# Optimization experiments

Hardware: AMD Instinct MI355X
Metric: run time of the kernel (lower is better)

## Reference

```python
import jax, jax.numpy as jnp
import numpy as np

# Dimensions: d_model D, heads H, head dim DH (H*DH==D), resonator freqs NF, FFN rank R
B, T, D, H, DH, NF, R = 2, 1024, 1024, 16, 64, 256, 4096
EPS_LN = 1e-5
EPS_ATTN = 1e-6


def setup_inputs() -> dict:
    key = jax.random.key(0)
    ks = jax.random.split(key, 16)
    n = lambda i, shape, s=0.02: jax.random.normal(ks[i], shape, dtype=jnp.float32) * s
    return {
        "x": jax.random.normal(ks[0], (B, T, D), dtype=jnp.float32),
        # resonator input projections
        "W_amp": n(1, (D, NF)), "b_amp": jnp.zeros((NF,), jnp.float32),
        "W_phi": n(2, (D, NF)), "b_phi": jnp.zeros((NF,), jnp.float32),
        # resonator dynamics: per-frequency rotation, retention logit, firing threshold
        "omega": jax.random.uniform(ks[3], (NF,), dtype=jnp.float32, minval=0.0, maxval=float(np.pi)),
        "ret_logit": jnp.full((NF,), 2.0, jnp.float32),
        "theta": jnp.full((NF,), 0.5, jnp.float32),
        # feat_proj: 3*NF -> D
        "W_feat": n(4, (3 * NF, D)), "b_feat": jnp.zeros((D,), jnp.float32),
        # linear attention projections (BDH-GPU style, relu feature map, no out proj)
        "Wq": n(5, (D, H * DH)), "Wk": n(6, (D, H * DH)), "Wv": n(7, (D, H * DH)),
        # per-head layernorm affine
        "lnh_w": jnp.ones((H, DH), jnp.float32), "lnh_b": jnp.zeros((H, DH), jnp.float32),
        # ReLU low-rank FFN (positive_out=True)
        "W1": n(8, (D, R)), "b1": jnp.zeros((R,), jnp.float32),
        "W2": n(9, (R, D)), "b2": jnp.zeros((D,), jnp.float32),
        # final layernorm
        "ln_w": jnp.ones((D,), jnp.float32), "ln_b": jnp.zeros((D,), jnp.float32),
    }


def reference(x, W_amp, b_amp, W_phi, b_phi, omega, ret_logit, theta,
              W_feat, b_feat, Wq, Wk, Wv, lnh_w, lnh_b,
              W1, b1, W2, b2, ln_w, ln_b):
    Bb, Tt, Dd = x.shape
    # --- resonator input field: complex polar(amp, phi) ---
    amp = jax.nn.softplus(x @ W_amp + b_amp)                 # [B,T,NF]
    phi = jnp.float32(np.pi) * jnp.tanh(x @ W_phi + b_phi)   # [B,T,NF]
    u = jax.lax.complex(amp * jnp.cos(phi), amp * jnp.sin(phi))  # complex64 [B,T,NF]
    # --- sequential complex resonator recurrence (the kernel-headroom scan) ---
    decay = jax.nn.sigmoid(ret_logit)                         # [NF]
    a = jax.lax.complex(decay * jnp.cos(omega), decay * jnp.sin(omega))  # [NF] complex

    def step(X, u_t):
        pre = a * X + u_t                                     # [B,NF] complex
        g = jax.nn.sigmoid(jnp.abs(pre) - theta)              # threshold-map gate
        Xn = pre * g.astype(pre.dtype)
        return Xn, Xn

    X0 = jnp.zeros((Bb, u.shape[-1]), jnp.complex64)
    _, Xs = jax.lax.scan(step, X0, jnp.swapaxes(u, 0, 1))     # [T,B,NF]
    Xs = jnp.swapaxes(Xs, 0, 1)                               # [B,T,NF]
    feat = jnp.concatenate([Xs.real, Xs.imag, jnp.abs(Xs)], axis=-1)  # [B,T,3NF]
    h = jax.nn.relu(feat @ W_feat + b_feat)                   # pos(feat_proj(feat)) -> [B,T,D]
    # --- causal linear attention (relu feature map, cumulative KV state) ---
    q = jax.nn.relu(h @ Wq).reshape(Bb, Tt, H, DH)
    k = jax.nn.relu(h @ Wk).reshape(Bb, Tt, H, DH)
    v = (h @ Wv).reshape(Bb, Tt, H, DH)
    kv = jnp.cumsum(k[..., :, None] * v[..., None, :], axis=1)  # [B,T,H,DH,DH]
    ksum = jnp.cumsum(k, axis=1)                                 # [B,T,H,DH]
    num = jnp.einsum('bthd,bthde->bthe', q, kv)
    den = jnp.einsum('bthd,bthd->bth', q, ksum)[..., None] + EPS_ATTN
    y = num / den                                                # [B,T,H,DH]
    # --- per-head layernorm ---
    mean = y.mean(-1, keepdims=True)
    var = y.var(-1, keepdims=True)
    y = (y - mean) / jnp.sqrt(var + EPS_LN) * lnh_w + lnh_b
    y = y.reshape(Bb, Tt, H * DH)                                # [B,T,D]
    # --- ReLU low-rank FFN, positive_out ---
    y = jax.nn.relu(jax.nn.relu(y @ W1 + b1) @ W2 + b2)
    # --- residual + layernorm ---
    z = x + y
    mu = z.mean(-1, keepdims=True)
    vz = z.var(-1, keepdims=True)
    out = (z - mu) / jnp.sqrt(vz + EPS_LN) * ln_w + ln_b
    return out
```

## Files before the change

kernel.cpp:

```cpp
#include <hip/hip_runtime.h>
#include <hip/hip_bf16.h>
#include <math.h>

#ifndef M_PI_F
#define M_PI_F 3.14159265358979323846f
#endif

static constexpr int Bb = 2, Tt = 1024, Dd = 1024, Hh = 16, DHh = 64, NFf = 256, Rr = 4096;
static constexpr int Mm = Bb * Tt;
static constexpr int CHK = 64, NCHK = Tt / CHK;
static constexpr int QS = 3072;

enum Epi { EPI_NONE = 0, EPI_RELU, EPI_QKV };

typedef __attribute__((ext_vector_type(8))) short bf16x8;
typedef __attribute__((ext_vector_type(4))) float f32x4;

__device__ inline float bf2f(unsigned short u) {
  union { unsigned int i; float f; } c;
  c.i = (unsigned int)u << 16;
  return c.f;
}

__device__ inline void gload16(const short* g, short* l) {
  __builtin_amdgcn_global_load_lds(
      (const __attribute__((address_space(1))) unsigned int*)g,
      (__attribute__((address_space(3))) unsigned int*)l, 16, 0, 0);
}

#define GSTAGE(bufsel, kk0)                                           \
  _Pragma("unroll") for (int si = 0; si < 4; ++si) {                  \
    const int s = wid + si * 4;                                       \
    gload16(A + (size_t)(m0 + s * 8 + srow) * ldk + (kk0) + skk,      \
            &lA[(bufsel) * 8192 + s * 512]);                          \
    gload16(BT + (size_t)(n0 + s * 8 + srow) * ldk + (kk0) + skk,     \
            &lB[(bufsel) * 8192 + s * 512]);                          \
  }

template <int EPI, int OUTBF, int SPLITK>
__global__ __launch_bounds__(256) void gemm_mfma(const short* __restrict__ A,
                                                 const short* __restrict__ BT,
                                                 const float* __restrict__ bias,
                                                 float* __restrict__ Cf,
                                                 __hip_bfloat16* __restrict__ Cb,
                                                 int M, int N, int ldk) {
  __shared__ short lA[2 * 128 * 64];
  __shared__ short lB[2 * 128 * 64];
  const int tid = threadIdx.x;
  const int wid = tid >> 6, lane = tid & 63;

  const int nwg = gridDim.x * gridDim.y;
  const int wg = blockIdx.y * gridDim.x + blockIdx.x;
  const int qq = nwg >> 3, rr = nwg & 7;
  const int xcd = wg & 7, idx = wg >> 3;
  const int wg2 = (xcd < rr ? xcd * (qq + 1) : rr * (qq + 1) + (xcd - rr) * qq) + idx;
  const int bx = wg2 % gridDim.x, by = wg2 / gridDim.x;

  const int m0 = by * 128, n0 = bx * 128;
  const int wm = (wid >> 1) * 64, wn = (wid & 1) * 64;
  const int srow = lane >> 3;
  const int skk = (((lane & 7) ^ (lane >> 3)) << 3);

  int kstart = 0, klen = ldk;
  if (SPLITK > 1) {
    klen = ldk / SPLITK;
    kstart = blockIdx.z * klen;
    if (OUTBF)
      Cb += (size_t)blockIdx.z * M * N;
    else
      Cf += (size_t)blockIdx.z * M * N;
  }
  const int kend = kstart + klen;

  f32x4 acc[4][4] = {};

  GSTAGE(0, kstart);
  int cur = 0;
  for (int k0 = kstart; k0 < kend; k0 += 64) {
    if (k0 + 64 < kend) {
      GSTAGE(cur ^ 1, k0 + 64);
      asm volatile("s_waitcnt vmcnt(8)" ::: "memory");
    } else {
      asm volatile("s_waitcnt vmcnt(0)" ::: "memory");
    }
    asm volatile("s_barrier" ::: "memory");
    const short* bA = &lA[cur * 8192];
    const short* bB = &lB[cur * 8192];
#pragma unroll
    for (int kk = 0; kk < 2; ++kk) {
      const int krd = kk * 32 + (lane >> 4) * 8;
      const int rsel = lane & 15;
      const int kswz = krd ^ ((rsel & 7) << 3);
      bf16x8 af[4], bfr[4];
#pragma unroll
      for (int i = 0; i < 4; ++i) {
        af[i] = *(const bf16x8*)&bA[(wm + i * 16 + rsel) * 64 + kswz];
        bfr[i] = *(const bf16x8*)&bB[(wn + i * 16 + rsel) * 64 + kswz];
      }
#pragma unroll
      for (int i = 0; i < 4; ++i)
#pragma unroll
        for (int j = 0; j < 4; ++j)
          acc[i][j] = __builtin_amdgcn_mfma_f32_16x16x32_bf16(af[i], bfr[j], acc[i][j], 0, 0, 0);
    }
    asm volatile("s_barrier" ::: "memory");
    cur ^= 1;
  }

  const int crow = (lane >> 4) * 4;
  const int ccol = lane & 15;
#pragma unroll
  for (int j = 0; j < 4; ++j) {
    const int col = n0 + wn + j * 16 + ccol;
    const float bv = bias ? bias[col] : 0.f;
#pragma unroll
    for (int i = 0; i < 4; ++i) {
#pragma unroll
      for (int r = 0; r < 4; ++r) {
        float v = acc[i][j][r] + bv;
        const int row = m0 + wm + i * 16 + crow + r;
        if (EPI == EPI_QKV) {
          const float vv = (col < 2048) ? fmaxf(v, 0.f) : v;
          Cb[(size_t)row * QS + col] = __float2bfloat16(vv);
        } else {
          if (EPI == EPI_RELU) v = fmaxf(v, 0.f);
          const size_t off = (size_t)row * N + col;
          if (OUTBF)
            Cb[off] = __float2bfloat16(v);
          else
            Cf[off] = v;
        }
      }
    }
  }
}

__device__ __forceinline__ void tc_tile(float (*tile)[33], const float* __restrict__ W,
                                        __hip_bfloat16* __restrict__ WT, int K, int N,
                                        int tlocal) {
  const int tilesN = N / 32;
  const int bk = (tlocal / tilesN) * 32, bn = (tlocal % tilesN) * 32;
  const int tx = threadIdx.x & 31, ty = threadIdx.x >> 5;
#pragma unroll
  for (int r = 0; r < 32; r += 8) tile[ty + r][tx] = W[(size_t)(bk + ty + r) * N + bn + tx];
  __syncthreads();
#pragma unroll
  for (int r = 0; r < 32; r += 8)
    WT[(size_t)(bn + ty + r) * K + bk + tx] = __float2bfloat16(tile[tx][ty + r]);
}

__global__ __launch_bounds__(256) void tc_first(const float* __restrict__ W_amp,
                                                const float* __restrict__ W_phi,
                                                __hip_bfloat16* __restrict__ WTamp,
                                                __hip_bfloat16* __restrict__ WTphi,
                                                const float* __restrict__ x,
                                                __hip_bfloat16* __restrict__ xb) {
  __shared__ float tile[32][33];
  const int bid = blockIdx.x;
  if (bid >= 512) {
    const int i = ((bid - 512) * 256 + threadIdx.x) * 4;
    const float4 v = *(const float4*)&x[i];
    xb[i + 0] = __float2bfloat16(v.x);
    xb[i + 1] = __float2bfloat16(v.y);
    xb[i + 2] = __float2bfloat16(v.z);
    xb[i + 3] = __float2bfloat16(v.w);
    return;
  }
  if (bid < 256)
    tc_tile(tile, W_amp, WTamp, 1024, 256, bid);
  else
    tc_tile(tile, W_phi, WTphi, 1024, 256, bid - 256);
}

__global__ __launch_bounds__(256) void reduce_polar(const __hip_bfloat16* __restrict__ part,
                                                    const float* __restrict__ b_amp,
                                                    const float* __restrict__ b_phi,
                                                    __hip_bfloat16* __restrict__ outr,
                                                    __hip_bfloat16* __restrict__ outi) {
  const int idx = blockIdx.x * 256 + threadIdx.x;
  const int row = idx >> 8, c = idx & 255;
  const size_t MN = (size_t)Mm * 512;
  const size_t pa = (size_t)row * 512 + c;
  const unsigned short* pu = (const unsigned short*)part;
  float a = bf2f(pu[pa]) + bf2f(pu[pa + MN]) + bf2f(pu[pa + 2 * MN]) + bf2f(pu[pa + 3 * MN]) +
            b_amp[c];
  float ph = bf2f(pu[pa + 256]) + bf2f(pu[pa + 256 + MN]) + bf2f(pu[pa + 256 + 2 * MN]) +
             bf2f(pu[pa + 256 + 3 * MN]) + b_phi[c];
  a = (a > 0.f) ? (a + log1pf(expf(-a))) : log1pf(expf(a));
  ph = M_PI_F * tanhf(ph);
  float s, co;
  sincosf(ph, &s, &co);
  outr[idx] = __float2bfloat16(a * co);
  outi[idx] = __float2bfloat16(a * s);
}

static constexpr int RES_P = 16;
static constexpr int RES_TC = 128;
static constexpr int RES_W = 128;

#define RES_LOAD(buf_r, buf_i, tg)                                        \
  if ((tg) < cend) {                                                      \
    _Pragma("unroll") for (int i = 0; i < RES_P; ++i) {                   \
      buf_r[i] = __bfloat162float(ur[bbase + (size_t)((tg) + i) * NFf]);  \
      buf_i[i] = __bfloat162float(ui[bbase + (size_t)((tg) + i) * NFf]);  \
    }                                                                     \
  }

#define RES_STEP(buf_r, buf_i, tg)                                      \
  {                                                                      \
    const bool wr_ = (tg) >= cstart;                                     \
    _Pragma("unroll") for (int i = 0; i < RES_P; ++i) {                  \
      const float pr = fmaf(ar, Xr, fmaf(-ai, Xi, buf_r[i]));            \
      const float pim = fmaf(ar, Xi, fmaf(ai, Xr, buf_i[i]));            \
      const float mag = __builtin_amdgcn_sqrtf(fmaf(pr, pr, pim * pim)); \
      const float g = __builtin_amdgcn_rcpf(1.f + __expf(th - mag));     \
      Xr = pr * g;                                                       \
      Xi = pim * g;                                                      \
      if (wr_) {                                                         \
        const size_t fb = ((size_t)b * Tt + (tg) + i) * (3 * NFf);       \
        featb[fb + f] = __float2bfloat16(Xr);                            \
        featb[fb + NFf + f] = __float2bfloat16(Xi);                      \
        featb[fb + 2 * NFf + f] = __float2bfloat16(mag * g);             \
      }                                                                  \
    }                                                                    \
  }

struct STDesc {
  const float* src[6];
  __hip_bfloat16* dst[6];
  const __hip_bfloat16* ur;
  const __hip_bfloat16* ui;
  const float* omega;
  const float* ret_logit;
  const float* theta;
  __hip_bfloat16* featb;
};

__global__ __launch_bounds__(256) void scan_and_tc(STDesc d) {
  __shared__ float tile[32][33];
  const int bid = blockIdx.x;
  if (bid < 64) {
    if (threadIdx.x >= 64) return;
    const int tc = bid & 7;
    const int fs = (bid >> 3) & 3;
    const int b = bid >> 5;
    const int f = fs * 64 + threadIdx.x;
    const int cstart = tc * RES_TC;
    const int cend = cstart + RES_TC;
    const int tbeg = (cstart >= RES_W) ? cstart - RES_W : 0;
    const __hip_bfloat16* ur = d.ur;
    const __hip_bfloat16* ui = d.ui;
    __hip_bfloat16* featb = d.featb;
    const float dec = 1.f / (1.f + __expf(-d.ret_logit[f]));
    float so, co;
    sincosf(d.omega[f], &so, &co);
    const float ar = dec * co, ai = dec * so;
    const float th = d.theta[f];
    const size_t bbase = (size_t)b * Tt * NFf + f;
    float Xr = 0.f, Xi = 0.f;
    float Ar[RES_P], Ai[RES_P], Br[RES_P], Bi[RES_P];
    RES_LOAD(Ar, Ai, tbeg);
    for (int t0 = tbeg; t0 < cend; t0 += 2 * RES_P) {
      RES_LOAD(Br, Bi, t0 + RES_P);
      RES_STEP(Ar, Ai, t0);
      RES_LOAD(Ar, Ai, t0 + 2 * RES_P);
      RES_STEP(Br, Bi, t0 + RES_P);
    }
    return;
  }
  constexpr int KS[6] = {768, 1024, 1024, 1024, 1024, 4096};
  constexpr int NS[6] = {1024, 1024, 1024, 1024, 4096, 1024};
  constexpr int CUM[7] = {0, 768, 1792, 2816, 3840, 7936, 12032};
  const int t = bid - 64;
  int w = 0;
#pragma unroll
  for (int i = 0; i < 6; ++i)
    if (t >= CUM[i + 1]) w = i + 1;
  tc_tile(tile, d.src[w], d.dst[w], KS[w], NS[w], t - CUM[w]);
}

__global__ __launch_bounds__(256) void attn_chunk_kv(const __hip_bfloat16* __restrict__ k,
                                                     const __hip_bfloat16* __restrict__ v,
                                                     __hip_bfloat16* __restrict__ S,
                                                     float* __restrict__ Ksum) {
  __shared__ float Ks[64][68], Vs[64][68];
  const int g = blockIdx.x;
  const int j = g & (NCHK - 1), bh = g >> 4;
  const int b = bh >> 4, h = bh & (Hh - 1);
  const int tid = threadIdx.x;
  const size_t rowbase = (size_t)(b * Tt + j * CHK) * QS + h * DHh;
  const unsigned short* ku = (const unsigned short*)k;
  const unsigned short* vu = (const unsigned short*)v;
  for (int l = tid; l < 4096; l += 256) {
    const int s = l >> 6, d = l & 63;
    Ks[s][d] = bf2f(ku[rowbase + (size_t)s * QS + d]);
    Vs[s][d] = bf2f(vu[rowbase + (size_t)s * QS + d]);
  }
  __syncthreads();
  const int d0 = tid & 63, eb = tid >> 6, e0 = eb * 16;
  float4 acc4[4] = {};
  float ks = 0.f;
  for (int s = 0; s < 64; ++s) {
    const float kd = Ks[s][d0];
    ks += kd;
#pragma unroll
    for (int i = 0; i < 4; ++i) {
      const float4 v4 = *(const float4*)&Vs[s][e0 + 4 * i];
      acc4[i].x = fmaf(kd, v4.x, acc4[i].x);
      acc4[i].y = fmaf(kd, v4.y, acc4[i].y);
      acc4[i].z = fmaf(kd, v4.z, acc4[i].z);
      acc4[i].w = fmaf(kd, v4.w, acc4[i].w);
    }
  }
  unsigned short* Sg = (unsigned short*)S + (size_t)g * 4096 + (size_t)d0 * 64 + e0;
#pragma unroll
  for (int i = 0; i < 4; ++i) {
    ushort4 o;
    __hip_bfloat16 h0 = __float2bfloat16(acc4[i].x);
    __hip_bfloat16 h1 = __float2bfloat16(acc4[i].y);
    __hip_bfloat16 h2 = __float2bfloat16(acc4[i].z);
    __hip_bfloat16 h3 = __float2bfloat16(acc4[i].w);
    o.x = *(unsigned short*)&h0;
    o.y = *(unsigned short*)&h1;
    o.z = *(unsigned short*)&h2;
    o.w = *(unsigned short*)&h3;
    *(ushort4*)&Sg[4 * i] = o;
  }
  if (eb == 0) Ksum[(size_t)g * 64 + d0] = ks;
}

__global__ __launch_bounds__(256) void attn_prefix(__hip_bfloat16* __restrict__ S,
                                                   float* __restrict__ Ksum) {
  const int bid = blockIdx.x;
  const int tid = threadIdx.x;
  if (bid < 512) {
    const int bh = bid >> 4, r = bid & 15;
    const int de = r * 256 + tid;
    unsigned short* Su = (unsigned short*)S;
    const size_t base = (size_t)bh * (NCHK * 4096) + de;
    float vv[NCHK];
#pragma unroll
    for (int j = 0; j < NCHK; ++j) vv[j] = bf2f(Su[base + (size_t)j * 4096]);
    float run = 0.f;
#pragma unroll
    for (int j = 0; j < NCHK; ++j) {
      const float tmp = vv[j];
      __hip_bfloat16 hv = __float2bfloat16(run);
      Su[base + (size_t)j * 4096] = *(unsigned short*)&hv;
      run += tmp;
    }
  } else {
    const int cid = (bid - 512) * 256 + tid;
    const int bh = cid >> 6, d = cid & 63;
    const size_t base = (size_t)bh * (NCHK * 64) + d;
    float vv[NCHK];
#pragma unroll
    for (int j = 0; j < NCHK; ++j) vv[j] = Ksum[base + (size_t)j * 64];
    float run = 0.f;
#pragma unroll
    for (int j = 0; j < NCHK; ++j) {
      const float tmp = vv[j];
      Ksum[base + (size_t)j * 64] = run;
      run += tmp;
    }
  }
}

__global__ __launch_bounds__(256) void attn_out(const __hip_bfloat16* __restrict__ q,
                                                const __hip_bfloat16* __restrict__ k,
                                                const __hip_bfloat16* __restrict__ v,
                                                const __hip_bfloat16* __restrict__ S,
                                                const float* __restrict__ Ksum,
                                                const float* __restrict__ lnw,
                                                const float* __restrict__ lnb,
                                                __hip_bfloat16* __restrict__ yhb) {
  __shared__ float Qs[64][68];
  __shared__ float KVP[64][68];
  __shared__ float At[64][66];
  __shared__ float denp[4][64];
  const int g = blockIdx.x;
  const int j = g & (NCHK - 1), bh = g >> 4;
  const int b = bh >> 4, h = bh & (Hh - 1);
  const int tid = threadIdx.x;
  const size_t rowbase = (size_t)(b * Tt + j * CHK) * QS + h * DHh;
  const unsigned short* qu = (const unsigned short*)q;
  const unsigned short* ku = (const unsigned short*)k;
  const unsigned short* vu = (const unsigned short*)v;
#define KSWZ(s, d) ((((d) >> 2) ^ (((s) >> 4) & 3)) * 4 + ((d) & 3))
  for (int l = tid; l < 4096; l += 256) {
    const int s = l >> 6, d = l & 63;
    Qs[s][d] = bf2f(qu[rowbase + (size_t)s * QS + d]);
    KVP[s][KSWZ(s, d)] = bf2f(vu[rowbase + (size_t)s * QS + d]);
  }
  {
    const int w4 = tid >> 6, ln = tid & 63;
    const int fr = ln & 15;
    const int kh = ln >> 4;
    const unsigned short* kr = ku + rowbase + (size_t)(w4 * 16 + fr) * QS + kh * 8;
    const bf16x8 a0 = *(const bf16x8*)&kr[0];
    const bf16x8 a1 = *(const bf16x8*)&kr[32];
    f32x4 accQK[4] = {};
#pragma unroll
    for (int tt = 0; tt < 4; ++tt) {
      const unsigned short* qr = qu + rowbase + (size_t)(tt * 16 + fr) * QS + kh * 8;
      const bf16x8 b0 = *(const bf16x8*)&qr[0];
      const bf16x8 b1 = *(const bf16x8*)&qr[32];
      accQK[tt] = __builtin_amdgcn_mfma_f32_16x16x32_bf16(a0, b0, accQK[tt], 0, 0, 0);
      accQK[tt] = __builtin_amdgcn_mfma_f32_16x16x32_bf16(a1, b1, accQK[tt], 0, 0, 0);
    }
#pragma unroll
    for (int tt = 0; tt < 4; ++tt) {
      const int t = tt * 16 + fr;
      float dp = 0.f;
#pragma unroll
      for (int r = 0; r < 4; ++r) {
        const int s = w4 * 16 + kh * 4 + r;
        const float val = (s <= t) ? accQK[tt][r] : 0.f;
        At[s][t] = val;
        dp += val;
      }
      dp += __shfl_xor(dp, 16);
      dp += __shfl_xor(dp, 32);
      if (ln < 16) denp[w4][t] = dp;
    }
  }
  __syncthreads();
  const int t = tid >> 2, sg = tid & 3;
  const float* pk = Ksum + (size_t)g * 64;
  float qpk = 0.f;
#pragma unroll
  for (int c = 0; c < 16; ++c) {
    const float4 q4 = *(const float4*)&Qs[t][4 * c];
    const float4 pk4 = *(const float4*)&pk[4 * c];
    qpk = fmaf(q4.x, pk4.x, fmaf(q4.y, pk4.y, fmaf(q4.z, pk4.z, fmaf(q4.w, pk4.w, qpk))));
  }
  const float den = denp[0][t] + denp[1][t] + denp[2][t] + denp[3][t] + qpk + 1e-6f;
  const int e0 = sg * 16;
  float4 num[4] = {};
  for (int s = 0; s <= t; ++s) {
    const float av = At[s][t];
    const int x = (s >> 4) & 3;
#pragma unroll
    for (int i = 0; i < 4; ++i) {
      const float4 v4 = *(const float4*)&KVP[s][e0 + 4 * (i ^ x)];
      num[i].x = fmaf(av, v4.x, num[i].x);
      num[i].y = fmaf(av, v4.y, num[i].y);
      num[i].z = fmaf(av, v4.z, num[i].z);
      num[i].w = fmaf(av, v4.w, num[i].w);
    }
  }
  __syncthreads();
  const unsigned short* Pg = (const unsigned short*)S + (size_t)g * 4096;
  for (int l = tid; l < 4096; l += 256) KVP[l >> 6][KSWZ(l >> 6, l & 63)] = bf2f(Pg[l]);
  __syncthreads();
  for (int d = 0; d < 64; ++d) {
    const float qd = Qs[t][d];
    const int x = (d >> 4) & 3;
#pragma unroll
    for (int i = 0; i < 4; ++i) {
      const float4 p4 = *(const float4*)&KVP[d][e0 + 4 * (i ^ x)];
      num[i].x = fmaf(qd, p4.x, num[i].x);
      num[i].y = fmaf(qd, p4.y, num[i].y);
      num[i].z = fmaf(qd, p4.z, num[i].z);
      num[i].w = fmaf(qd, p4.w, num[i].w);
    }
  }
#undef KSWZ
  const float inv = 1.f / den;
  float o[16];
#pragma unroll
  for (int i = 0; i < 4; ++i) {
    o[4 * i + 0] = num[i].x * inv;
    o[4 * i + 1] = num[i].y * inv;
    o[4 * i + 2] = num[i].z * inv;
    o[4 * i + 3] = num[i].w * inv;
  }
  float s1 = 0.f, s2 = 0.f;
#pragma unroll
  for (int i = 0; i < 16; ++i) {
    s1 += o[i];
    s2 += o[i] * o[i];
  }
  s1 += __shfl_xor(s1, 1);
  s1 += __shfl_xor(s1, 2);
  s2 += __shfl_xor(s2, 1);
  s2 += __shfl_xor(s2, 2);
  const float mean = s1 * (1.f / 64.f);
  const float var = s2 * (1.f / 64.f) - mean * mean;
  const float rsv = rsqrtf(var + 1e-5f);
  const float* wv = lnw + h * DHh + e0;
  const float* bv = lnb + h * DHh + e0;
  unsigned short ob[16];
#pragma unroll
  for (int i = 0; i < 16; ++i) {
    const float r = (o[i] - mean) * rsv * wv[i] + bv[i];
    __hip_bfloat16 hv = __float2bfloat16(r);
    ob[i] = *(unsigned short*)&hv;
  }
  unsigned short* yg =
      (unsigned short*)yhb + (size_t)(b * Tt + j * CHK + t) * Dd + h * DHh + e0;
#pragma unroll
  for (int i = 0; i < 4; ++i) *(ushort4*)&yg[4 * i] = *(ushort4*)&ob[4 * i];
}

__global__ __launch_bounds__(256) void final_ln(const float* __restrict__ x,
                                                const __hip_bfloat16* __restrict__ part,
                                                const float* __restrict__ b2,
                                                const float* __restrict__ w,
                                                const float* __restrict__ bb,
                                                float* __restrict__ out) {
  __shared__ float r1[4], r2[4];
  const int row = blockIdx.x;
  const int tid = threadIdx.x;
  const size_t off = (size_t)row * Dd + tid * 4;
  const size_t MN = (size_t)Mm * Dd;
  float acc4[4] = {0.f, 0.f, 0.f, 0.f};
#pragma unroll
  for (int z = 0; z < 4; ++z) {
    const ushort4 u = *(const ushort4*)&part[off + (size_t)z * MN];
    acc4[0] += bf2f(u.x);
    acc4[1] += bf2f(u.y);
    acc4[2] += bf2f(u.z);
    acc4[3] += bf2f(u.w);
  }
  const float4 bv = *(const float4*)&b2[tid * 4];
  const float4 xa = *(const float4*)&x[off];
  float z[4];
  z[0] = xa.x + fmaxf(acc4[0] + bv.x, 0.f);
  z[1] = xa.y + fmaxf(acc4[1] + bv.y, 0.f);
  z[2] = xa.z + fmaxf(acc4[2] + bv.z, 0.f);
  z[3] = xa.w + fmaxf(acc4[3] + bv.w, 0.f);
  float s1 = z[0] + z[1] + z[2] + z[3];
  float s2 = z[0] * z[0] + z[1] * z[1] + z[2] * z[2] + z[3] * z[3];
#pragma unroll
  for (int o = 1; o < 64; o <<= 1) {
    s1 += __shfl_xor(s1, o);
    s2 += __shfl_xor(s2, o);
  }
  const int wid = tid >> 6;
  if ((tid & 63) == 0) {
    r1[wid] = s1;
    r2[wid] = s2;
  }
  __syncthreads();
  const float t1 = r1[0] + r1[1] + r1[2] + r1[3];
  const float t2 = r2[0] + r2[1] + r2[2] + r2[3];
  const float mu = t1 * (1.f / Dd);
  const float var = t2 * (1.f / Dd) - mu * mu;
  const float rsv = rsqrtf(var + 1e-5f);
  float4 o4;
  float* op = &o4.x;
#pragma unroll
  for (int jj = 0; jj < 4; ++jj) op[jj] = (z[jj] - mu) * rsv * w[tid * 4 + jj] + bb[tid * 4 + jj];
  *(float4*)&out[off] = o4;
}

extern "C" void kernel_launch(void* const* d_in, const int* in_sizes, int n_in,
                              void* d_out, int out_size, void* d_ws, size_t ws_size,
                              hipStream_t stream) {
  const float* x = (const float*)d_in[0];
  const float* W_amp = (const float*)d_in[1];
  const float* b_amp = (const float*)d_in[2];
  const float* W_phi = (const float*)d_in[3];
  const float* b_phi = (const float*)d_in[4];
  const float* omega = (const float*)d_in[5];
  const float* ret_logit = (const float*)d_in[6];
  const float* theta = (const float*)d_in[7];
  const float* W_feat = (const float*)d_in[8];
  const float* b_feat = (const float*)d_in[9];
  const float* Wq = (const float*)d_in[10];
  const float* Wk = (const float*)d_in[11];
  const float* Wv = (const float*)d_in[12];
  const float* lnh_w = (const float*)d_in[13];
  const float* lnh_b = (const float*)d_in[14];
  const float* W1 = (const float*)d_in[15];
  const float* b1 = (const float*)d_in[16];
  const float* W2 = (const float*)d_in[17];
  const float* b2 = (const float*)d_in[18];
  const float* ln_w = (const float*)d_in[19];
  const float* ln_b = (const float*)d_in[20];

  char* p = (char*)d_ws;
  auto alloc = [&](size_t bytes) {
    char* r = p;
    p += (bytes + 255) & ~(size_t)255;
    return r;
  };
  __hip_bfloat16* xb = (__hip_bfloat16*)alloc((size_t)Mm * Dd * 2);
  __hip_bfloat16* urh = (__hip_bfloat16*)alloc((size_t)Mm * NFf * 2);
  __hip_bfloat16* uih = (__hip_bfloat16*)alloc((size_t)Mm * NFf * 2);
  __hip_bfloat16* WTamp = (__hip_bfloat16*)alloc((size_t)NFf * Dd * 2);
  __hip_bfloat16* WTphi = (__hip_bfloat16*)alloc((size_t)NFf * Dd * 2);
  __hip_bfloat16* WTfeat = (__hip_bfloat16*)alloc((size_t)Dd * 3 * NFf * 2);
  __hip_bfloat16* WTq = (__hip_bfloat16*)alloc((size_t)Dd * Dd * 2);
  __hip_bfloat16* WTk = (__hip_bfloat16*)alloc((size_t)Dd * Dd * 2);
  __hip_bfloat16* WTv = (__hip_bfloat16*)alloc((size_t)Dd * Dd * 2);
  __hip_bfloat16* WT1 = (__hip_bfloat16*)alloc((size_t)Rr * Dd * 2);
  __hip_bfloat16* WT2 = (__hip_bfloat16*)alloc((size_t)Dd * Rr * 2);
  __hip_bfloat16* hb = (__hip_bfloat16*)alloc((size_t)Mm * Dd * 2);
  __hip_bfloat16* qkvb = (__hip_bfloat16*)alloc((size_t)Mm * QS * 2);
  __hip_bfloat16* yhb = (__hip_bfloat16*)alloc((size_t)Mm * Dd * 2);
  __hip_bfloat16* S = (__hip_bfloat16*)alloc((size_t)Bb * Hh * NCHK * 4096 * 2);
  float* Ksum = (float*)alloc((size_t)Bb * Hh * NCHK * 64 * 4);
  __hip_bfloat16* f1b = (__hip_bfloat16*)alloc((size_t)Mm * Rr * 2);
  __hip_bfloat16* pamp = (__hip_bfloat16*)alloc((size_t)4 * Mm * 512 * 2);
  __hip_bfloat16* pffn2 = (__hip_bfloat16*)alloc((size_t)4 * Mm * Dd * 2);

  __hip_bfloat16* featb = xb;
  const __hip_bfloat16* q = qkvb;
  const __hip_bfloat16* k = qkvb + 1024;
  const __hip_bfloat16* v = qkvb + 2048;
  float* out = (float*)d_out;

  const dim3 blk(256);

  tc_first<<<dim3(2560), blk, 0, stream>>>(W_amp, W_phi, WTamp, WTphi, x, xb);

  gemm_mfma<EPI_NONE, 1, 4><<<dim3(512 / 128, Mm / 128, 4), blk, 0, stream>>>(
      (const short*)xb, (const short*)WTamp, nullptr, nullptr, pamp, Mm, 512, Dd);
  reduce_polar<<<dim3(Mm * NFf / 256), blk, 0, stream>>>(pamp, b_amp, b_phi, urh, uih);

  STDesc st;
  st.src[0] = W_feat; st.dst[0] = WTfeat;
  st.src[1] = Wq; st.dst[1] = WTq;
  st.src[2] = Wk; st.dst[2] = WTk;
  st.src[3] = Wv; st.dst[3] = WTv;
  st.src[4] = W1; st.dst[4] = WT1;
  st.src[5] = W2; st.dst[5] = WT2;
  st.ur = urh; st.ui = uih;
  st.omega = omega; st.ret_logit = ret_logit; st.theta = theta;
  st.featb = featb;
  scan_and_tc<<<dim3(64 + 12032), blk, 0, stream>>>(st);

  gemm_mfma<EPI_RELU, 1, 0><<<dim3(Dd / 128, Mm / 128), blk, 0, stream>>>(
      (const short*)featb, (const short*)WTfeat, b_feat, nullptr, hb, Mm, Dd, 3 * NFf);

  gemm_mfma<EPI_QKV, 1, 0><<<dim3(QS / 128, Mm / 128), blk, 0, stream>>>(
      (const short*)hb, (const short*)WTq, nullptr, nullptr, qkvb, Mm, QS, Dd);

  attn_chunk_kv<<<dim3(Bb * Hh * NCHK), blk, 0, stream>>>(k, v, S, Ksum);
  attn_prefix<<<dim3(520), blk, 0, stream>>>(S, Ksum);
  attn_out<<<dim3(Bb * Hh * NCHK), blk, 0, stream>>>(q, k, v, S, Ksum, lnh_w, lnh_b, yhb);

  gemm_mfma<EPI_RELU, 1, 0><<<dim3(Rr / 128, Mm / 128), blk, 0, stream>>>(
      (const short*)yhb, (const short*)WT1, b1, nullptr, f1b, Mm, Rr, Dd);

  gemm_mfma<EPI_NONE, 1, 4><<<dim3(Dd / 128, Mm / 128, 4), blk, 0, stream>>>(
      (const short*)f1b, (const short*)WT2, nullptr, nullptr, pffn2, Mm, Dd, Rr);

  final_ln<<<dim3(Mm), blk, 0, stream>>>(x, pffn2, b2, ln_w, ln_b, out);
}
```

Before: 171.4 us.

## Compute attention chunk output with bf16 MFMA using split hi/lo scores

The attn_out kernel replaces its scalar FP32 intra-chunk (A·V) and inter-chunk (Q·P) accumulation loops with bf16 MFMA 16x16x32 instructions. V and the prefix state are stored transposed in LDS as bf16. The score matrix is split into a high and a low bf16 part so the A·V product keeps near-FP32 accuracy. The per-head layernorm moves into the MFMA output layout with wider shuffle reductions, and the denominators are computed cooperatively. This removes a large amount of VALU FMA work and LDS traffic, at the cost of extra MFMAs and scattered 2-byte output stores.

```diff
diff --git a/kernel.cpp b/kernel.cpp
--- a/kernel.cpp
+++ b/kernel.cpp
@@ -20,6 +20,11 @@
   union { unsigned int i; float f; } c;
   c.i = (unsigned int)u << 16;
   return c.f;
+}
+
+__device__ inline unsigned short f2bf(float f) {
+  __hip_bfloat16 h = __float2bfloat16(f);
+  return *(unsigned short*)&h;
 }
 
 __device__ inline void gload16(const short* g, short* l) {
@@ -316,14 +321,10 @@
 #pragma unroll
   for (int i = 0; i < 4; ++i) {
     ushort4 o;
-    __hip_bfloat16 h0 = __float2bfloat16(acc4[i].x);
-    __hip_bfloat16 h1 = __float2bfloat16(acc4[i].y);
-    __hip_bfloat16 h2 = __float2bfloat16(acc4[i].z);
-    __hip_bfloat16 h3 = __float2bfloat16(acc4[i].w);
-    o.x = *(unsigned short*)&h0;
-    o.y = *(unsigned short*)&h1;
-    o.z = *(unsigned short*)&h2;
-    o.w = *(unsigned short*)&h3;
+    o.x = f2bf(acc4[i].x);
+    o.y = f2bf(acc4[i].y);
+    o.z = f2bf(acc4[i].z);
+    o.w = f2bf(acc4[i].w);
     *(ushort4*)&Sg[4 * i] = o;
   }
   if (eb == 0) Ksum[(size_t)g * 64 + d0] = ks;
@@ -345,8 +346,7 @@
 #pragma unroll
     for (int j = 0; j < NCHK; ++j) {
       const float tmp = vv[j];
-      __hip_bfloat16 hv = __float2bfloat16(run);
-      Su[base + (size_t)j * 4096] = *(unsigned short*)&hv;
+      Su[base + (size_t)j * 4096] = f2bf(run);
       run += tmp;
     }
   } else {
@@ -374,10 +374,12 @@
                                                 const float* __restrict__ lnw,
                                                 const float* __restrict__ lnb,
                                                 __hip_bfloat16* __restrict__ yhb) {
-  __shared__ float Qs[64][68];
-  __shared__ float KVP[64][68];
-  __shared__ float At[64][66];
+  __shared__ unsigned short Atb[64][72];
+  __shared__ unsigned short Atl[64][72];
+  __shared__ unsigned short Vt[64][72];
+  __shared__ unsigned short Pt[64][72];
   __shared__ float denp[4][64];
+  __shared__ float dens[64];
   const int g = blockIdx.x;
   const int j = g & (NCHK - 1), bh = g >> 4;
   const int b = bh >> 4, h = bh & (Hh - 1);
@@ -386,11 +388,12 @@
   const unsigned short* qu = (const unsigned short*)q;
   const unsigned short* ku = (const unsigned short*)k;
   const unsigned short* vu = (const unsigned short*)v;
-#define KSWZ(s, d) ((((d) >> 2) ^ (((s) >> 4) & 3)) * 4 + ((d) & 3))
+  const unsigned short* Pg = (const unsigned short*)S + (size_t)g * 4096;
+
   for (int l = tid; l < 4096; l += 256) {
-    const int s = l >> 6, d = l & 63;
-    Qs[s][d] = bf2f(qu[rowbase + (size_t)s * QS + d]);
-    KVP[s][KSWZ(s, d)] = bf2f(vu[rowbase + (size_t)s * QS + d]);
+    const int s = l >> 6, e = l & 63;
+    Vt[e][s] = vu[rowbase + (size_t)s * QS + e];
+    Pt[e][s] = Pg[l];
   }
   {
     const int w4 = tid >> 6, ln = tid & 63;
@@ -416,7 +419,9 @@
       for (int r = 0; r < 4; ++r) {
         const int s = w4 * 16 + kh * 4 + r;
         const float val = (s <= t) ? accQK[tt][r] : 0.f;
-        At[s][t] = val;
+        const unsigned short hv = f2bf(val);
+        Atb[t][s] = hv;
+        Atl[t][s] = f2bf(val - bf2f(hv));
         dp += val;
       }
       dp += __shfl_xor(dp, 16);
@@ -425,82 +430,72 @@
     }
   }
   __syncthreads();
-  const int t = tid >> 2, sg = tid & 3;
-  const float* pk = Ksum + (size_t)g * 64;
-  float qpk = 0.f;
-#pragma unroll
-  for (int c = 0; c < 16; ++c) {
-    const float4 q4 = *(const float4*)&Qs[t][4 * c];
-    const float4 pk4 = *(const float4*)&pk[4 * c];
-    qpk = fmaf(q4.x, pk4.x, fmaf(q4.y, pk4.y, fmaf(q4.z, pk4.z, fmaf(q4.w, pk4.w, qpk))));
-  }
-  const float den = denp[0][t] + denp[1][t] + denp[2][t] + denp[3][t] + qpk + 1e-6f;
-  const int e0 = sg * 16;
-  float4 num[4] = {};
-  for (int s = 0; s <= t; ++s) {
-    const float av = At[s][t];
-    const int x = (s >> 4) & 3;
-#pragma unroll
-    for (int i = 0; i < 4; ++i) {
-      const float4 v4 = *(const float4*)&KVP[s][e0 + 4 * (i ^ x)];
-      num[i].x = fmaf(av, v4.x, num[i].x);
-      num[i].y = fmaf(av, v4.y, num[i].y);
-      num[i].z = fmaf(av, v4.z, num[i].z);
-      num[i].w = fmaf(av, v4.w, num[i].w);
-    }
+  {
+    const int t = tid >> 2, sg = tid & 3;
+    const float* pk = Ksum + (size_t)g * 64;
+    const unsigned short* qr = qu + rowbase + (size_t)t * QS + sg * 16;
+    float qpk = 0.f;
+#pragma unroll
+    for (int i = 0; i < 16; ++i) qpk = fmaf(bf2f(qr[i]), pk[sg * 16 + i], qpk);
+    qpk += __shfl_xor(qpk, 1);
+    qpk += __shfl_xor(qpk, 2);
+    if (sg == 0)
+      dens[t] = denp[0][t] + denp[1][t] + denp[2][t] + denp[3][t] + qpk + 1e-6f;
   }
   __syncthreads();
-  const unsigned short* Pg = (const unsigned short*)S + (size_t)g * 4096;
-  for (int l = tid; l < 4096; l += 256) KVP[l >> 6][KSWZ(l >> 6, l & 63)] = bf2f(Pg[l]);
-  __syncthreads();
-  for (int d = 0; d < 64; ++d) {
-    const float qd = Qs[t][d];
-    const int x = (d >> 4) & 3;
-#pragma unroll
-    for (int i = 0; i < 4; ++i) {
-      const float4 p4 = *(const float4*)&KVP[d][e0 + 4 * (i ^ x)];
-      num[i].x = fmaf(qd, p4.x, num[i].x);
-      num[i].y = fmaf(qd, p4.y, num[i].y);
-      num[i].z = fmaf(qd, p4.z, num[i].z);
-      num[i].w = fmaf(qd, p4.w, num[i].w);
-    }
-  }
-#undef KSWZ
-  const float inv = 1.f / den;
-  float o[16];
-#pragma unroll
-  for (int i = 0; i < 4; ++i) {
-    o[4 * i + 0] = num[i].x * inv;
-    o[4 * i + 1] = num[i].y * inv;
-    o[4 * i + 2] = num[i].z * inv;
-    o[4 * i + 3] = num[i].w * inv;
-  }
-  float s1 = 0.f, s2 = 0.f;
-#pragma unroll
-  for (int i = 0; i < 16; ++i) {
-    s1 += o[i];
-    s2 += o[i] * o[i];
-  }
-  s1 += __shfl_xor(s1, 1);
-  s1 += __shfl_xor(s1, 2);
-  s2 += __shfl_xor(s2, 1);
-  s2 += __shfl_xor(s2, 2);
-  const float mean = s1 * (1.f / 64.f);
-  const float var = s2 * (1.f / 64.f) - mean * mean;
-  const float rsv = rsqrtf(var + 1e-5f);
-  const float* wv = lnw + h * DHh + e0;
-  const float* bv = lnb + h * DHh + e0;
-  unsigned short ob[16];
-#pragma unroll
-  for (int i = 0; i < 16; ++i) {
-    const float r = (o[i] - mean) * rsv * wv[i] + bv[i];
-    __hip_bfloat16 hv = __float2bfloat16(r);
-    ob[i] = *(unsigned short*)&hv;
-  }
-  unsigned short* yg =
-      (unsigned short*)yhb + (size_t)(b * Tt + j * CHK + t) * Dd + h * DHh + e0;
-#pragma unroll
-  for (int i = 0; i < 4; ++i) *(ushort4*)&yg[4 * i] = *(ushort4*)&ob[4 * i];
+  const int w = tid >> 6, ln = tid & 63;
+  const int fr = ln & 15;
+  const int kh = ln >> 4;
+  const bf16x8 sa0 = *(const bf16x8*)&Atb[w * 16 + fr][kh * 8];
+  const bf16x8 sa1 = *(const bf16x8*)&Atb[w * 16 + fr][kh * 8 + 32];
+  const bf16x8 la0 = *(const bf16x8*)&Atl[w * 16 + fr][kh * 8];
+  const bf16x8 la1 = *(const bf16x8*)&Atl[w * 16 + fr][kh * 8 + 32];
+  const unsigned short* q2 = qu + rowbase + (size_t)(w * 16 + fr) * QS + kh * 8;
+  const bf16x8 qa0 = *(const bf16x8*)&q2[0];
+  const bf16x8 qa1 = *(const bf16x8*)&q2[32];
+  f32x4 acc2[4] = {};
+#pragma unroll
+  for (int ct = 0; ct < 4; ++ct) {
+    const bf16x8 vb0 = *(const bf16x8*)&Vt[ct * 16 + fr][kh * 8];
+    const bf16x8 vb1 = *(const bf16x8*)&Vt[ct * 16 + fr][kh * 8 + 32];
+    const bf16x8 pb0 = *(const bf16x8*)&Pt[ct * 16 + fr][kh * 8];
+    const bf16x8 pb1 = *(const bf16x8*)&Pt[ct * 16 + fr][kh * 8 + 32];
+    acc2[ct] = __builtin_amdgcn_mfma_f32_16x16x32_bf16(sa0, vb0, acc2[ct], 0, 0, 0);
+    acc2[ct] = __builtin_amdgcn_mfma_f32_16x16x32_bf16(sa1, vb1, acc2[ct], 0, 0, 0);
+    acc2[ct] = __builtin_amdgcn_mfma_f32_16x16x32_bf16(la0, vb0, acc2[ct], 0, 0, 0);
+    acc2[ct] = __builtin_amdgcn_mfma_f32_16x16x32_bf16(la1, vb1, acc2[ct], 0, 0, 0);
+    acc2[ct] = __builtin_amdgcn_mfma_f32_16x16x32_bf16(qa0, pb0, acc2[ct], 0, 0, 0);
+    acc2[ct] = __builtin_amdgcn_mfma_f32_16x16x32_bf16(qa1, pb1, acc2[ct], 0, 0, 0);
+  }
+  unsigned short* yb = (unsigned short*)yhb;
+#pragma unroll
+  for (int r = 0; r < 4; ++r) {
+    const int t = w * 16 + kh * 4 + r;
+    const float inv = 1.f / dens[t];
+    float o[4];
+    float s1 = 0.f, s2 = 0.f;
+#pragma unroll
+    for (int ct = 0; ct < 4; ++ct) {
+      o[ct] = acc2[ct][r] * inv;
+      s1 += o[ct];
+      s2 += o[ct] * o[ct];
+    }
+#pragma unroll
+    for (int m = 1; m < 16; m <<= 1) {
+      s1 += __shfl_xor(s1, m);
+      s2 += __shfl_xor(s2, m);
+    }
+    const float mean = s1 * (1.f / 64.f);
+    const float var = s2 * (1.f / 64.f) - mean * mean;
+    const float rsv = rsqrtf(var + 1e-5f);
+    unsigned short* yg = yb + (size_t)(b * Tt + j * CHK + t) * Dd + h * DHh;
+#pragma unroll
+    for (int ct = 0; ct < 4; ++ct) {
+      const int e = ct * 16 + fr;
+      const float rr = (o[ct] - mean) * rsv * lnw[h * DHh + e] + lnb[h * DHh + e];
+      yg[e] = f2bf(rr);
+    }
+  }
 }
 
 __global__ __launch_bounds__(256) void final_ln(const float* __restrict__ x,
```

Result: faster. 159.5 us (-6.9%).
